# Kernel tuning notes

Hardware: AMD Instinct MI355X
Metric: run time of the kernel (lower is better)

The kernel has to match this reference:

```python
import jax, jax.numpy as jnp
import numpy as np
from jax import lax

EPS = 1e-5

def ste_sign(x):
    # forward-only module: plain sign is fine
    return jnp.sign(x)

def conv2d(x, w, pad):
    # x: NCHW, w: OIHW, stride 1
    return lax.conv_general_dilated(x, w, window_strides=(1, 1),
                                    padding=[(pad, pad), (pad, pad)],
                                    dimension_numbers=('NCHW', 'OIHW', 'NCHW'))

def maxpool2(x):
    # 2x2 max pool, stride 2, VALID (floor) -- matches nn.MaxPool2d(2,2)
    return lax.reduce_window(x, -jnp.inf, lax.max, (1, 1, 2, 2), (1, 1, 2, 2), 'VALID')

def batchnorm(x, gamma, beta):
    # training-mode BN: batch statistics over (N,H,W), biased variance
    mean = jnp.mean(x, axis=(0, 2, 3), keepdims=True)
    var = jnp.var(x, axis=(0, 2, 3), keepdims=True)
    xn = (x - mean) * lax.rsqrt(var + EPS)
    return xn * gamma[None, :, None, None] + beta[None, :, None, None]

def setup_inputs() -> dict:
    key = jax.random.key(0)
    ks = jax.random.split(key, 8)
    def he(k, shape):
        n = shape[2] * shape[3] * shape[0]
        return jax.random.normal(k, shape, jnp.float32) * np.sqrt(2.0 / n)
    x = jax.random.normal(ks[0], (4096, 1, 28, 28), jnp.float32)
    w0 = he(ks[1], (32, 1, 3, 3))
    w1 = he(ks[2], (32, 32, 3, 3))
    w2 = he(ks[3], (32, 32, 3, 3))
    g0 = jnp.ones((32,), jnp.float32); b0 = jnp.zeros((32,), jnp.float32)
    g1 = jnp.ones((32,), jnp.float32); b1 = jnp.zeros((32,), jnp.float32)
    g2 = jnp.ones((32,), jnp.float32); b2 = jnp.zeros((32,), jnp.float32)
    fw = jax.random.normal(ks[4], (10, 288), jnp.float32) * 0.01
    fb = jnp.zeros((10,), jnp.float32)
    return {"x": x, "w0": w0, "g0": g0, "b0": b0, "w1": w1, "g1": g1, "b1": b1,
            "w2": w2, "g2": g2, "b2": b2, "fw": fw, "fb": fb}

def reference(x, w0, g0, b0, w1, g1, b1, w2, g2, b2, fw, fb):
    # block0: fp conv -> pool -> bn (no act)
    h = batchnorm(maxpool2(conv2d(x, w0, 1)), g0, b0)          # [B,32,14,14]
    # block1: binary(1w1a) conv -> pool -> bn + maxpool(shortcut)
    o = batchnorm(maxpool2(conv2d(ste_sign(h), ste_sign(w1), 1)), g1, b1)
    h = o + maxpool2(h)                                         # [B,32,7,7]
    # block2
    o = batchnorm(maxpool2(conv2d(ste_sign(h), ste_sign(w2), 1)), g2, b2)
    h = o + maxpool2(h)                                         # [B,32,3,3]
    h = h.reshape(h.shape[0], -1)                                # [B,288]
    return h @ fw.T + fb                                         # [B,10]
```

## Files before the change

### kernel.cpp

```cpp
#include <hip/hip_runtime.h>
#include <stdint.h>

#define BATCH 4096

typedef float v16f __attribute__((ext_vector_type(16)));
typedef short v8s  __attribute__((ext_vector_type(8)));

__device__ __forceinline__ int sgn8(float v) {
    return (v > 0.f) ? 1 : ((v < 0.f) ? -1 : 0);
}

__global__ void k_signw1(const float* __restrict__ w, uint16_t* __restrict__ o) {
    int i = blockIdx.x * 256 + threadIdx.x;
    if (i >= 9216) return;
    int j = i & 7, n = (i >> 3) & 31, q = (i >> 8) & 1, kh = (i >> 9) & 1, tp = i >> 10;
    int cin = kh * 16 + q * 8 + j;
    float v = w[(n * 32 + cin) * 9 + tp];
    o[i] = (v > 0.f) ? 0x3F80 : ((v < 0.f) ? 0xBF80 : 0);
}

__global__ __launch_bounds__(448) void k_conv0s(const float* __restrict__ x,
                                                const float* __restrict__ w0,
                                                double* __restrict__ part0) {
    __shared__ float xs[960];
    __shared__ float wl[288];
    __shared__ double rs[32][14], rq[32][14];
    int n = blockIdx.x, t = threadIdx.x;
    for (int i = t; i < 960; i += 448) xs[i] = 0.f;
    for (int i = t; i < 288; i += 448) wl[i] = w0[i];
    __syncthreads();
    for (int i = t; i < 784; i += 448) {
        int y = i / 28, xx = i - y * 28;
        xs[(y + 1) * 32 + xx + 1] = x[n * 784 + i];
    }
    __syncthreads();
    int c = t & 31, py = t >> 5;
    float wreg[9];
    #pragma unroll
    for (int i = 0; i < 9; ++i) wreg[i] = wl[c * 9 + i];
    const float4* X4 = (const float4*)xs;
    float4 cur0 = X4[(2 * py + 0) * 8];
    float4 cur1 = X4[(2 * py + 1) * 8];
    float4 cur2 = X4[(2 * py + 2) * 8];
    float4 cur3 = X4[(2 * py + 3) * 8];
    double s = 0.0, q = 0.0;
    #pragma unroll
    for (int k = 0; k < 7; ++k) {
        float4 n0 = X4[(2 * py + 0) * 8 + k + 1];
        float4 n1 = X4[(2 * py + 1) * 8 + k + 1];
        float4 n2 = X4[(2 * py + 2) * 8 + k + 1];
        float4 n3 = X4[(2 * py + 3) * 8 + k + 1];
        float a[4][6];
        a[0][0] = cur0.x; a[0][1] = cur0.y; a[0][2] = cur0.z; a[0][3] = cur0.w; a[0][4] = n0.x; a[0][5] = n0.y;
        a[1][0] = cur1.x; a[1][1] = cur1.y; a[1][2] = cur1.z; a[1][3] = cur1.w; a[1][4] = n1.x; a[1][5] = n1.y;
        a[2][0] = cur2.x; a[2][1] = cur2.y; a[2][2] = cur2.z; a[2][3] = cur2.w; a[2][4] = n2.x; a[2][5] = n2.y;
        a[3][0] = cur3.x; a[3][1] = cur3.y; a[3][2] = cur3.z; a[3][3] = cur3.w; a[3][4] = n3.x; a[3][5] = n3.y;
        #pragma unroll
        for (int e = 0; e < 2; ++e) {
            int base = 2 * e;
            float s00 = 0.f, s01 = 0.f, s10 = 0.f, s11 = 0.f;
            #pragma unroll
            for (int ky = 0; ky < 3; ++ky)
            #pragma unroll
            for (int kx = 0; kx < 3; ++kx) {
                float w = wreg[ky * 3 + kx];
                s00 = fmaf(a[ky][base + kx], w, s00);
                s01 = fmaf(a[ky][base + kx + 1], w, s01);
                s10 = fmaf(a[ky + 1][base + kx], w, s10);
                s11 = fmaf(a[ky + 1][base + kx + 1], w, s11);
            }
            float m = fmaxf(fmaxf(s00, s01), fmaxf(s10, s11));
            double v = (double)m;
            s += v; q += v * v;
        }
        cur0 = n0; cur1 = n1; cur2 = n2; cur3 = n3;
    }
    rs[c][py] = s; rq[c][py] = q;
    __syncthreads();
    if (t < 32) {
        double S = 0.0, Q = 0.0;
        #pragma unroll
        for (int i = 0; i < 14; ++i) { S += rs[t][i]; Q += rq[t][i]; }
        part0[(size_t)t * 4096 + n] = S;
        part0[(size_t)32 * 4096 + (size_t)t * 4096 + n] = Q;
    }
}

__global__ __launch_bounds__(256) void k_finalize(const double* __restrict__ part, int G,
                                                  const float* __restrict__ g,
                                                  const float* __restrict__ b,
                                                  double inv_count, float* __restrict__ ss) {
    int c = blockIdx.x, t = threadIdx.x;
    double s = 0.0, q = 0.0;
    for (int i = t; i < G; i += 256) {
        s += part[(size_t)c * G + i];
        q += part[(size_t)32 * G + (size_t)c * G + i];
    }
    #pragma unroll
    for (int o = 32; o > 0; o >>= 1) { s += __shfl_down(s, o); q += __shfl_down(q, o); }
    __shared__ double rs[4], rq[4];
    int w = t >> 6, l = t & 63;
    if (l == 0) { rs[w] = s; rq[w] = q; }
    __syncthreads();
    if (t == 0) {
        s = rs[0] + rs[1] + rs[2] + rs[3];
        q = rq[0] + rq[1] + rq[2] + rq[3];
        double mean = s * inv_count;
        double var = q * inv_count - mean * mean;
        double sc = (double)g[c] / sqrt(var + 1e-5);
        ss[c] = (float)sc;
        ss[32 + c] = (float)((double)b[c] - mean * sc);
    }
}

__global__ __launch_bounds__(448) void k_bn0r(const float* __restrict__ x,
                                              const float* __restrict__ w0,
                                              const float* __restrict__ ss,
                                              uint32_t* __restrict__ s0b,
                                              float* __restrict__ hp0) {
    __shared__ float xs[960];
    __shared__ float wl[288];
    __shared__ float P[6468];
    int n = blockIdx.x, t = threadIdx.x;
    for (int i = t; i < 960; i += 448) xs[i] = 0.f;
    for (int i = t; i < 288; i += 448) wl[i] = w0[i];
    __syncthreads();
    for (int i = t; i < 784; i += 448) {
        int y = i / 28, xx = i - y * 28;
        xs[(y + 1) * 32 + xx + 1] = x[n * 784 + i];
    }
    __syncthreads();
    int c = t & 31, py = t >> 5;
    float wreg[9];
    #pragma unroll
    for (int i = 0; i < 9; ++i) wreg[i] = wl[c * 9 + i];
    float sc = ss[c], sh = ss[32 + c];
    const float4* X4 = (const float4*)xs;
    float4 cur0 = X4[(2 * py + 0) * 8];
    float4 cur1 = X4[(2 * py + 1) * 8];
    float4 cur2 = X4[(2 * py + 2) * 8];
    float4 cur3 = X4[(2 * py + 3) * 8];
    #pragma unroll
    for (int k = 0; k < 7; ++k) {
        float4 n0 = X4[(2 * py + 0) * 8 + k + 1];
        float4 n1 = X4[(2 * py + 1) * 8 + k + 1];
        float4 n2 = X4[(2 * py + 2) * 8 + k + 1];
        float4 n3 = X4[(2 * py + 3) * 8 + k + 1];
        float a[4][6];
        a[0][0] = cur0.x; a[0][1] = cur0.y; a[0][2] = cur0.z; a[0][3] = cur0.w; a[0][4] = n0.x; a[0][5] = n0.y;
        a[1][0] = cur1.x; a[1][1] = cur1.y; a[1][2] = cur1.z; a[1][3] = cur1.w; a[1][4] = n1.x; a[1][5] = n1.y;
        a[2][0] = cur2.x; a[2][1] = cur2.y; a[2][2] = cur2.z; a[2][3] = cur2.w; a[2][4] = n2.x; a[2][5] = n2.y;
        a[3][0] = cur3.x; a[3][1] = cur3.y; a[3][2] = cur3.z; a[3][3] = cur3.w; a[3][4] = n3.x; a[3][5] = n3.y;
        #pragma unroll
        for (int e = 0; e < 2; ++e) {
            int base = 2 * e;
            float s00 = 0.f, s01 = 0.f, s10 = 0.f, s11 = 0.f;
            #pragma unroll
            for (int ky = 0; ky < 3; ++ky)
            #pragma unroll
            for (int kx = 0; kx < 3; ++kx) {
                float w = wreg[ky * 3 + kx];
                s00 = fmaf(a[ky][base + kx], w, s00);
                s01 = fmaf(a[ky][base + kx + 1], w, s01);
                s10 = fmaf(a[ky + 1][base + kx], w, s10);
                s11 = fmaf(a[ky + 1][base + kx + 1], w, s11);
            }
            float m = fmaxf(fmaxf(s00, s01), fmaxf(s10, s11));
            P[(py * 14 + 2 * k + e) * 33 + c] = fmaf(sc, m, sh);
        }
        cur0 = n0; cur1 = n1; cur2 = n2; cur3 = n3;
    }
    __syncthreads();
    uint32_t* simg = s0b + (size_t)n * 4096;
    for (int i = t; i < 784; i += 448) {
        int pl = i >> 2, qd = i & 3;
        int iy = pl / 14, ix = pl - iy * 14;
        int yy = iy + 1, xx2 = ix + 1;
        int p = yy * 16 + xx2;
        int psw = (xx2 & 3) ^ (yy & 3);
        int g = qd ^ psw;
        const float* Pp = &P[pl * 33 + g * 8];
        uint32_t d[4];
        #pragma unroll
        for (int j = 0; j < 4; ++j) {
            float h0 = Pp[2 * j], h1 = Pp[2 * j + 1];
            uint32_t b0 = (h0 > 0.f) ? 0x3F80u : ((h0 < 0.f) ? 0xBF80u : 0u);
            uint32_t b1 = (h1 > 0.f) ? 0x3F80u : ((h1 < 0.f) ? 0xBF80u : 0u);
            d[j] = b0 | (b1 << 16);
        }
        uint4 v; v.x = d[0]; v.y = d[1]; v.z = d[2]; v.w = d[3];
        *(uint4*)(simg + p * 16 + qd * 4) = v;
    }
    if (t < 240) {
        int e = t >> 2, qd = t & 3;
        int yh, xh;
        if (e < 16)      { yh = 0;      xh = e; }
        else if (e < 32) { yh = 15;     xh = e - 16; }
        else if (e < 46) { yh = e - 31; xh = 0; }
        else             { yh = e - 45; xh = 15; }
        uint4 z; z.x = z.y = z.z = z.w = 0u;
        *(uint4*)(simg + (yh * 16 + xh) * 16 + qd * 4) = z;
    }
    if (t < 196) {
        int pw = t >> 2, oct = t & 3;
        int pyy = pw / 7, pxx = pw - pyy * 7;
        int b00 = ((2 * pyy) * 14 + 2 * pxx) * 33;
        int b01 = b00 + 33;
        int b10 = b00 + 14 * 33;
        int b11 = b10 + 33;
        float out[8];
        #pragma unroll
        for (int k = 0; k < 8; ++k) {
            int cc = oct * 8 + k;
            out[k] = fmaxf(fmaxf(P[b00 + cc], P[b01 + cc]),
                           fmaxf(P[b10 + cc], P[b11 + cc]));
        }
        float4* hd = (float4*)(hp0 + ((size_t)n * 49 + pw) * 32 + oct * 8);
        float4 h0; h0.x = out[0]; h0.y = out[1]; h0.z = out[2]; h0.w = out[3];
        float4 h1; h1.x = out[4]; h1.y = out[5]; h1.z = out[6]; h1.w = out[7];
        hd[0] = h0; hd[1] = h1;
    }
}

__global__ __launch_bounds__(256) void k_conv1m(const uint32_t* __restrict__ s0b,
                                                const uint16_t* __restrict__ w1f,
                                                float* __restrict__ p1,
                                                double* __restrict__ part1) {
    __shared__ uint32_t lds[8192];
    int t = threadIdx.x;
    int n0 = blockIdx.x * 2;
    const uint4* gp = (const uint4*)(s0b + (size_t)n0 * 4096);
    uint4* lp = (uint4*)lds;
    #pragma unroll
    for (int i = 0; i < 8; ++i) lp[t + i * 256] = gp[t + i * 256];
    int lane = t & 63, wv = t >> 6;
    int q = lane >> 5, ncol = lane & 31;
    v8s wfr[18];
    #pragma unroll
    for (int f = 0; f < 18; ++f)
        wfr[f] = *(const v8s*)(w1f + (f * 2 + q) * 256 + ncol * 8);
    __syncthreads();
    int img = wv >> 1, wh = wv & 1;
    int n = n0 + img;
    int ibase = img * 4096;
    int m = lane & 31;
    int quad = m & 3, pwl = m >> 2;
    int dy = quad >> 1, dx = quad & 1;
    double sAcc = 0.0, qAcc = 0.0;
    for (int tile = wh; tile < 7; tile += 2) {
        int pw = tile * 8 + pwl;
        int pwc = min(pw, 48);
        int py = pwc / 7, px = pwc - py * 7;
        int pbase = (2 * py + dy) * 16 + 2 * px + dx;
        v16f acc;
        #pragma unroll
        for (int i = 0; i < 16; ++i) acc[i] = 0.f;
        #pragma unroll
        for (int tp = 0; tp < 9; ++tp) {
            int p = pbase + (tp / 3) * 16 + (tp % 3);
            int psw = (p ^ (p >> 4)) & 3;
            #pragma unroll
            for (int kh = 0; kh < 2; ++kh) {
                int g = kh * 2 + q;
                int idx = ibase + p * 16 + ((g ^ psw) << 2);
                v8s a = *(const v8s*)&lds[idx];
                acc = __builtin_amdgcn_mfma_f32_32x32x16_bf16(a, wfr[tp * 2 + kh], acc, 0, 0, 0);
            }
        }
        #pragma unroll
        for (int g4 = 0; g4 < 4; ++g4) {
            float mx = fmaxf(fmaxf(acc[4 * g4], acc[4 * g4 + 1]),
                             fmaxf(acc[4 * g4 + 2], acc[4 * g4 + 3]));
            int pwo = tile * 8 + 2 * g4 + q;
            if (pwo < 49) {
                p1[((size_t)n * 49 + pwo) * 32 + ncol] = mx;
                double v = (double)mx;
                sAcc += v; qAcc += v * v;
            }
        }
    }
    __syncthreads();
    double* red = (double*)lds;
    red[(wv * 2 + q) * 32 + ncol] = sAcc;
    red[256 + (wv * 2 + q) * 32 + ncol] = qAcc;
    __syncthreads();
    if (t < 32) {
        double S = 0.0, Q = 0.0;
        #pragma unroll
        for (int i = 0; i < 8; ++i) { S += red[i * 32 + t]; Q += red[256 + i * 32 + t]; }
        part1[(size_t)t * 2048 + blockIdx.x] = S;
        part1[(size_t)32 * 2048 + (size_t)t * 2048 + blockIdx.x] = Q;
    }
}

__global__ __launch_bounds__(256) void k_bn1(const float* __restrict__ p1,
                                             const float* __restrict__ hp0,
                                             const float* __restrict__ ss,
                                             uint32_t* __restrict__ s1,
                                             float* __restrict__ hp1) {
    __shared__ float H[1568];
    int n = blockIdx.x, t = threadIdx.x;
    const float* P = p1 + (size_t)n * 1568;
    const float* Hp = hp0 + (size_t)n * 1568;
    for (int i = t; i < 1568; i += 256) {
        int c = i & 31;
        H[i] = fmaf(ss[64 + c], P[i], ss[96 + c]) + Hp[i];
    }
    __syncthreads();
    if (t < 32) {
        int c = t;
        uint32_t* sp = s1 + (size_t)n * 416 + c * 13;
        for (int j = 0; j < 13; ++j) {
            uint32_t u = 0;
            #pragma unroll
            for (int k = 0; k < 4; ++k) {
                int f = 4 * j + k;
                int sv = (f < 49) ? sgn8(H[f * 32 + c]) : 0;
                u |= ((uint32_t)(uint8_t)(int8_t)sv) << (8 * k);
            }
            sp[j] = u;
        }
    }
    for (int jj = t; jj < 288; jj += 256) {
        int c = jj / 9, pix = jj - c * 9;
        int r = pix / 3, qq = pix - r * 3;
        float a0 = H[((2 * r) * 7 + 2 * qq) * 32 + c];
        float a1 = H[((2 * r) * 7 + 2 * qq + 1) * 32 + c];
        float a2 = H[((2 * r + 1) * 7 + 2 * qq) * 32 + c];
        float a3 = H[((2 * r + 1) * 7 + 2 * qq + 1) * 32 + c];
        hp1[n * 288 + c * 9 + pix] = fmaxf(fmaxf(a0, a1), fmaxf(a2, a3));
    }
}

__global__ __launch_bounds__(256) void k_conv2m(const uint32_t* __restrict__ s1,
                                                const uint16_t* __restrict__ w2f,
                                                float* __restrict__ p2,
                                                double* __restrict__ part2) {
    __shared__ uint32_t lds[8192];
    int t = threadIdx.x;
    int n0 = blockIdx.x * 8;
    for (int i = t; i < 120; i += 256) {
        int img = i / 15, e = i - img * 15;
        int p = (e < 8) ? e : (e - 7) * 8;
        uint32_t* d = &lds[img * 1024 + p * 16];
        uint4 z; z.x = z.y = z.z = z.w = 0u;
        ((uint4*)d)[0] = z; ((uint4*)d)[1] = z; ((uint4*)d)[2] = z; ((uint4*)d)[3] = z;
    }
    int lane = t & 63, wv = t >> 6;
    int q = lane >> 5, ncol = lane & 31;
    v8s wfr[18];
    #pragma unroll
    for (int f = 0; f < 18; ++f)
        wfr[f] = *(const v8s*)(w2f + (f * 2 + q) * 256 + ncol * 8);
    for (int i = t; i < 1664; i += 256) {
        int img = i / 208, r = i - img * 208;
        int c2 = r / 13, j = r - c2 * 13;
        const uint32_t* sb = s1 + (size_t)(n0 + img) * 416;
        uint32_t wa = sb[(2 * c2) * 13 + j];
        uint32_t wb = sb[(2 * c2 + 1) * 13 + j];
        int g = c2 >> 2, sub = c2 & 3;
        #pragma unroll
        for (int k = 0; k < 4; ++k) {
            int f = 4 * j + k;
            if (f < 49) {
                int y = f / 7, x = f - y * 7;
                int p = (y + 1) * 8 + (x + 1);
                uint32_t ba = (wa >> (8 * k)) & 0xFF;
                uint32_t bb = (wb >> (8 * k)) & 0xFF;
                uint32_t ha = ba ? (0x3F80u | ((ba & 0x80u) << 8)) : 0u;
                uint32_t hb = bb ? (0x3F80u | ((bb & 0x80u) << 8)) : 0u;
                lds[img * 1024 + p * 16 + ((g ^ (p & 3)) << 2) + sub] = ha | (hb << 16);
            }
        }
    }
    __syncthreads();
    int m = lane & 31;
    int quad = m & 3, pwl = m >> 2;
    int dy = quad >> 1, dx = quad & 1;
    double sAcc = 0.0, qAcc = 0.0;
    for (int tile = wv; tile < 9; tile += 4) {
        int pwg = tile * 8 + pwl;
        int img = pwg / 9, pwi = pwg - img * 9;
        int py = pwi / 3, px = pwi - py * 3;
        int pbase = (2 * py + dy) * 8 + 2 * px + dx;
        v16f acc;
        #pragma unroll
        for (int i = 0; i < 16; ++i) acc[i] = 0.f;
        #pragma unroll
        for (int tp = 0; tp < 9; ++tp) {
            int p = pbase + (tp / 3) * 8 + (tp % 3);
            int psw = p & 3;
            #pragma unroll
            for (int kh = 0; kh < 2; ++kh) {
                int g = kh * 2 + q;
                int idx = img * 1024 + p * 16 + ((g ^ psw) << 2);
                v8s a = *(const v8s*)&lds[idx];
                acc = __builtin_amdgcn_mfma_f32_32x32x16_bf16(a, wfr[tp * 2 + kh], acc, 0, 0, 0);
            }
        }
        #pragma unroll
        for (int g4 = 0; g4 < 4; ++g4) {
            float mx = fmaxf(fmaxf(acc[4 * g4], acc[4 * g4 + 1]),
                             fmaxf(acc[4 * g4 + 2], acc[4 * g4 + 3]));
            int pwo = tile * 8 + 2 * g4 + q;
            int oimg = pwo / 9, opwi = pwo - oimg * 9;
            p2[(size_t)(n0 + oimg) * 288 + ncol * 9 + opwi] = mx;
            double v = (double)mx;
            sAcc += v; qAcc += v * v;
        }
    }
    __syncthreads();
    double* red = (double*)lds;
    red[(wv * 2 + q) * 32 + ncol] = sAcc;
    red[256 + (wv * 2 + q) * 32 + ncol] = qAcc;
    __syncthreads();
    if (t < 32) {
        double S = 0.0, Q = 0.0;
        #pragma unroll
        for (int i = 0; i < 8; ++i) { S += red[i * 32 + t]; Q += red[256 + i * 32 + t]; }
        part2[(size_t)t * 512 + blockIdx.x] = S;
        part2[(size_t)32 * 512 + (size_t)t * 512 + blockIdx.x] = Q;
    }
}

__global__ __launch_bounds__(256) void k_fc(const float* __restrict__ p2,
                                            const float* __restrict__ hp1,
                                            const float* __restrict__ ss,
                                            const float* __restrict__ fw,
                                            const float* __restrict__ fb,
                                            float* __restrict__ outv) {
    int wv = threadIdx.x >> 6, l = threadIdx.x & 63;
    int n = blockIdx.x * 4 + wv;
    float acc[10];
    #pragma unroll
    for (int k = 0; k < 10; ++k) acc[k] = 0.f;
    #pragma unroll
    for (int i = 0; i < 5; ++i) {
        int j = l + 64 * i;
        if (j < 288) {
            int c = j / 9;
            float h = fmaf(ss[128 + c], p2[n * 288 + j], ss[160 + c]) + hp1[n * 288 + j];
            #pragma unroll
            for (int k = 0; k < 10; ++k)
                acc[k] = fmaf(h, fw[k * 288 + j], acc[k]);
        }
    }
    #pragma unroll
    for (int k = 0; k < 10; ++k) {
        float s = acc[k];
        #pragma unroll
        for (int o = 32; o > 0; o >>= 1) s += __shfl_down(s, o);
        if (l == 0) outv[n * 10 + k] = s + fb[k];
    }
}

extern "C" void kernel_launch(void* const* d_in, const int* in_sizes, int n_in,
                              void* d_out, int out_size, void* d_ws, size_t ws_size,
                              hipStream_t stream) {
    (void)in_sizes; (void)n_in; (void)out_size; (void)ws_size;
    const float* x  = (const float*)d_in[0];
    const float* w0 = (const float*)d_in[1];
    const float* g0 = (const float*)d_in[2];
    const float* b0 = (const float*)d_in[3];
    const float* w1 = (const float*)d_in[4];
    const float* g1 = (const float*)d_in[5];
    const float* b1 = (const float*)d_in[6];
    const float* w2 = (const float*)d_in[7];
    const float* g2 = (const float*)d_in[8];
    const float* b2 = (const float*)d_in[9];
    const float* fw = (const float*)d_in[10];
    const float* fb = (const float*)d_in[11];
    float* outv = (float*)d_out;
    char* ws = (char*)d_ws;

    float*     ss    = (float*)(ws + 1024);
    uint16_t*  w1f   = (uint16_t*)(ws + 2048);
    uint16_t*  w2f   = (uint16_t*)(ws + 38912);
    float*     p1    = (float*)(ws + 76800);
    uint32_t*  s1    = (uint32_t*)(ws + 25766912);
    float*     hp1   = (float*)(ws + 32582656);
    float*     p2    = (float*)(ws + 37301248);
    uint32_t*  s0b   = (uint32_t*)(ws + 42019840);
    double*    part0 = (double*)(ws + 109128704);
    double*    part1 = (double*)(ws + 111225856);
    double*    part2 = (double*)(ws + 112274432);
    float*     hp0   = (float*)(ws + 128527360);

    k_signw1<<<36, 256, 0, stream>>>(w1, w1f);
    k_signw1<<<36, 256, 0, stream>>>(w2, w2f);

    k_conv0s<<<BATCH, 448, 0, stream>>>(x, w0, part0);
    k_finalize<<<32, 256, 0, stream>>>(part0, 4096, g0, b0, 1.0 / (BATCH * 196.0), ss);
    k_bn0r<<<BATCH, 448, 0, stream>>>(x, w0, ss, s0b, hp0);

    k_conv1m<<<BATCH / 2, 256, 0, stream>>>(s0b, w1f, p1, part1);
    k_finalize<<<32, 256, 0, stream>>>(part1, 2048, g1, b1, 1.0 / (BATCH * 49.0), ss + 64);
    k_bn1<<<BATCH, 256, 0, stream>>>(p1, hp0, ss, s1, hp1);

    k_conv2m<<<BATCH / 8, 256, 0, stream>>>(s1, w2f, p2, part2);
    k_finalize<<<32, 256, 0, stream>>>(part2, 512, g2, b2, 1.0 / (BATCH * 9.0), ss + 128);

    k_fc<<<BATCH / 4, 256, 0, stream>>>(p2, hp1, ss, fw, fb, outv);
}
```

Measured before the change: 217.9 us.

## Fold BN finalize into conv kernels via last-block atomic ticket

Drops the three separate finalize launches and the two weight-sign launches. The weight-sign work moves into the first conv kernel, and each conv kernel's last block, found with an atomic counter, computes the BN scale and shift. This cuts launch and serialization overhead, but the final statistics reduction now runs on a single block, looping over 32 channels serially with syncs. It also adds a memset to clear the counters.

After: 667.1 us. 3.06x slower.

```diff
diff --git a/kernel.cpp b/kernel.cpp
--- a/kernel.cpp
+++ b/kernel.cpp
@@ -10,22 +10,65 @@
     return (v > 0.f) ? 1 : ((v < 0.f) ? -1 : 0);
 }
 
-__global__ void k_signw1(const float* __restrict__ w, uint16_t* __restrict__ o) {
-    int i = blockIdx.x * 256 + threadIdx.x;
-    if (i >= 9216) return;
-    int j = i & 7, n = (i >> 3) & 31, q = (i >> 8) & 1, kh = (i >> 9) & 1, tp = i >> 10;
-    int cin = kh * 16 + q * 8 + j;
-    float v = w[(n * 32 + cin) * 9 + tp];
-    o[i] = (v > 0.f) ? 0x3F80 : ((v < 0.f) ? 0xBF80 : 0);
+__device__ void finalize_all(const double* __restrict__ part, int G,
+                             const float* __restrict__ g, const float* __restrict__ b,
+                             double inv_count, float* __restrict__ ssout,
+                             int t, double* red) {
+    for (int c = 0; c < 32; ++c) {
+        double s = 0.0, q = 0.0;
+        if (t < 256) {
+            for (int i = t; i < G; i += 256) {
+                s += part[(size_t)c * G + i];
+                q += part[(size_t)32 * G + (size_t)c * G + i];
+            }
+        }
+        #pragma unroll
+        for (int o = 32; o > 0; o >>= 1) { s += __shfl_down(s, o); q += __shfl_down(q, o); }
+        int w = t >> 6, l = t & 63;
+        if (l == 0 && w < 4) { red[w] = s; red[8 + w] = q; }
+        __syncthreads();
+        if (t == 0) {
+            s = red[0] + red[1] + red[2] + red[3];
+            q = red[8] + red[9] + red[10] + red[11];
+            double mean = s * inv_count;
+            double var = q * inv_count - mean * mean;
+            double sc = (double)g[c] / sqrt(var + 1e-5);
+            ssout[c] = (float)sc;
+            ssout[32 + c] = (float)((double)b[c] - mean * sc);
+        }
+        __syncthreads();
+    }
 }
 
 __global__ __launch_bounds__(448) void k_conv0s(const float* __restrict__ x,
                                                 const float* __restrict__ w0,
-                                                double* __restrict__ part0) {
+                                                const float* __restrict__ w1,
+                                                const float* __restrict__ w2,
+                                                const float* __restrict__ g0,
+                                                const float* __restrict__ b0,
+                                                uint16_t* __restrict__ w1f,
+                                                uint16_t* __restrict__ w2f,
+                                                double* __restrict__ part0,
+                                                float* __restrict__ ss,
+                                                uint32_t* __restrict__ counter) {
     __shared__ float xs[960];
     __shared__ float wl[288];
-    __shared__ double rs[32][14], rq[32][14];
+    __shared__ double rs[448], rq[448];
+    __shared__ double red[16];
+    __shared__ int isLast;
     int n = blockIdx.x, t = threadIdx.x;
+
+    if (n < 72 && t < 256) {
+        int i = n * 256 + t;
+        int ii = (i < 9216) ? i : i - 9216;
+        const float* w = (i < 9216) ? w1 : w2;
+        uint16_t* o = (i < 9216) ? w1f : w2f;
+        int j = ii & 7, nn = (ii >> 3) & 31, q2 = (ii >> 8) & 1, kh = (ii >> 9) & 1, tp = ii >> 10;
+        int cin = kh * 16 + q2 * 8 + j;
+        float v = w[(nn * 32 + cin) * 9 + tp];
+        o[ii] = (v > 0.f) ? 0x3F80 : ((v < 0.f) ? 0xBF80 : 0);
+    }
+
     for (int i = t; i < 960; i += 448) xs[i] = 0.f;
     for (int i = t; i < 288; i += 448) wl[i] = w0[i];
     __syncthreads();
@@ -75,41 +118,25 @@
         }
         cur0 = n0; cur1 = n1; cur2 = n2; cur3 = n3;
     }
-    rs[c][py] = s; rq[c][py] = q;
+    rs[c * 14 + py] = s; rq[c * 14 + py] = q;
     __syncthreads();
     if (t < 32) {
         double S = 0.0, Q = 0.0;
         #pragma unroll
-        for (int i = 0; i < 14; ++i) { S += rs[t][i]; Q += rq[t][i]; }
+        for (int i = 0; i < 14; ++i) { S += rs[t * 14 + i]; Q += rq[t * 14 + i]; }
         part0[(size_t)t * 4096 + n] = S;
         part0[(size_t)32 * 4096 + (size_t)t * 4096 + n] = Q;
-    }
-}
-
-__global__ __launch_bounds__(256) void k_finalize(const double* __restrict__ part, int G,
-                                                  const float* __restrict__ g,
-                                                  const float* __restrict__ b,
-                                                  double inv_count, float* __restrict__ ss) {
-    int c = blockIdx.x, t = threadIdx.x;
-    double s = 0.0, q = 0.0;
-    for (int i = t; i < G; i += 256) {
-        s += part[(size_t)c * G + i];
-        q += part[(size_t)32 * G + (size_t)c * G + i];
-    }
-    #pragma unroll
-    for (int o = 32; o > 0; o >>= 1) { s += __shfl_down(s, o); q += __shfl_down(q, o); }
-    __shared__ double rs[4], rq[4];
-    int w = t >> 6, l = t & 63;
-    if (l == 0) { rs[w] = s; rq[w] = q; }
+        __threadfence();
+    }
     __syncthreads();
     if (t == 0) {
-        s = rs[0] + rs[1] + rs[2] + rs[3];
-        q = rq[0] + rq[1] + rq[2] + rq[3];
-        double mean = s * inv_count;
-        double var = q * inv_count - mean * mean;
-        double sc = (double)g[c] / sqrt(var + 1e-5);
-        ss[c] = (float)sc;
-        ss[32 + c] = (float)((double)b[c] - mean * sc);
+        uint32_t ticket = atomicAdd(counter, 1u);
+        isLast = (ticket == (uint32_t)(gridDim.x - 1));
+    }
+    __syncthreads();
+    if (isLast) {
+        __threadfence();
+        finalize_all(part0, 4096, g0, b0, 1.0 / (4096.0 * 196.0), ss, t, red);
     }
 }
 
@@ -224,9 +251,14 @@
 
 __global__ __launch_bounds__(256) void k_conv1m(const uint32_t* __restrict__ s0b,
                                                 const uint16_t* __restrict__ w1f,
+                                                const float* __restrict__ g1,
+                                                const float* __restrict__ b1,
                                                 float* __restrict__ p1,
-                                                double* __restrict__ part1) {
+                                                double* __restrict__ part1,
+                                                float* __restrict__ ss,
+                                                uint32_t* __restrict__ counter) {
     __shared__ uint32_t lds[8192];
+    __shared__ int isLast;
     int t = threadIdx.x;
     int n0 = blockIdx.x * 2;
     const uint4* gp = (const uint4*)(s0b + (size_t)n0 * 4096);
@@ -290,6 +322,17 @@
         for (int i = 0; i < 8; ++i) { S += red[i * 32 + t]; Q += red[256 + i * 32 + t]; }
         part1[(size_t)t * 2048 + blockIdx.x] = S;
         part1[(size_t)32 * 2048 + (size_t)t * 2048 + blockIdx.x] = Q;
+        __threadfence();
+    }
+    __syncthreads();
+    if (t == 0) {
+        uint32_t ticket = atomicAdd(counter, 1u);
+        isLast = (ticket == (uint32_t)(gridDim.x - 1));
+    }
+    __syncthreads();
+    if (isLast) {
+        __threadfence();
+        finalize_all(part1, 2048, g1, b1, 1.0 / (4096.0 * 49.0), ss + 64, t, red + 512);
     }
 }
 
@@ -334,9 +377,14 @@
 
 __global__ __launch_bounds__(256) void k_conv2m(const uint32_t* __restrict__ s1,
                                                 const uint16_t* __restrict__ w2f,
+                                                const float* __restrict__ g2,
+                                                const float* __restrict__ b2,
                                                 float* __restrict__ p2,
-                                                double* __restrict__ part2) {
+                                                double* __restrict__ part2,
+                                                float* __restrict__ ss,
+                                                uint32_t* __restrict__ counter) {
     __shared__ uint32_t lds[8192];
+    __shared__ int isLast;
     int t = threadIdx.x;
     int n0 = blockIdx.x * 8;
     for (int i = t; i < 120; i += 256) {
@@ -363,8 +411,8 @@
         for (int k = 0; k < 4; ++k) {
             int f = 4 * j + k;
             if (f < 49) {
-                int y = f / 7, x = f - y * 7;
-                int p = (y + 1) * 8 + (x + 1);
+                int y = f / 7, xq = f - y * 7;
+                int p = (y + 1) * 8 + (xq + 1);
                 uint32_t ba = (wa >> (8 * k)) & 0xFF;
                 uint32_t bb = (wb >> (8 * k)) & 0xFF;
                 uint32_t ha = ba ? (0x3F80u | ((ba & 0x80u) << 8)) : 0u;
@@ -420,6 +468,17 @@
         for (int i = 0; i < 8; ++i) { S += red[i * 32 + t]; Q += red[256 + i * 32 + t]; }
         part2[(size_t)t * 512 + blockIdx.x] = S;
         part2[(size_t)32 * 512 + (size_t)t * 512 + blockIdx.x] = Q;
+        __threadfence();
+    }
+    __syncthreads();
+    if (t == 0) {
+        uint32_t ticket = atomicAdd(counter, 1u);
+        isLast = (ticket == (uint32_t)(gridDim.x - 1));
+    }
+    __syncthreads();
+    if (isLast) {
+        __threadfence();
+        finalize_all(part2, 512, g2, b2, 1.0 / (4096.0 * 9.0), ss + 128, t, red + 512);
     }
 }
 
@@ -473,6 +532,7 @@
     float* outv = (float*)d_out;
     char* ws = (char*)d_ws;
 
+    uint32_t*  ctr   = (uint32_t*)(ws + 0);
     float*     ss    = (float*)(ws + 1024);
     uint16_t*  w1f   = (uint16_t*)(ws + 2048);
     uint16_t*  w2f   = (uint16_t*)(ws + 38912);
@@ -486,19 +546,16 @@
     double*    part2 = (double*)(ws + 112274432);
     float*     hp0   = (float*)(ws + 128527360);
 
-    k_signw1<<<36, 256, 0, stream>>>(w1, w1f);
-    k_signw1<<<36, 256, 0, stream>>>(w2, w2f);
-
-    k_conv0s<<<BATCH, 448, 0, stream>>>(x, w0, part0);
-    k_finalize<<<32, 256, 0, stream>>>(part0, 4096, g0, b0, 1.0 / (BATCH * 196.0), ss);
+    hipMemsetAsync(ctr, 0, 64, stream);
+
+    k_conv0s<<<BATCH, 448, 0, stream>>>(x, w0, w1, w2, g0, b0, w1f, w2f,
+                                        part0, ss, ctr + 0);
     k_bn0r<<<BATCH, 448, 0, stream>>>(x, w0, ss, s0b, hp0);
 
-    k_conv1m<<<BATCH / 2, 256, 0, stream>>>(s0b, w1f, p1, part1);
-    k_finalize<<<32, 256, 0, stream>>>(part1, 2048, g1, b1, 1.0 / (BATCH * 49.0), ss + 64);
+    k_conv1m<<<BATCH / 2, 256, 0, stream>>>(s0b, w1f, g1, b1, p1, part1, ss, ctr + 1);
     k_bn1<<<BATCH, 256, 0, stream>>>(p1, hp0, ss, s1, hp1);
 
-    k_conv2m<<<BATCH / 8, 256, 0, stream>>>(s1, w2f, p2, part2);
-    k_finalize<<<32, 256, 0, stream>>>(part2, 512, g2, b2, 1.0 / (BATCH * 9.0), ss + 128);
+    k_conv2m<<<BATCH / 8, 256, 0, stream>>>(s1, w2f, g2, b2, p2, part2, ss, ctr + 2);
 
     k_fc<<<BATCH / 4, 256, 0, stream>>>(p2, hp1, ss, fw, fb, outv);
 }
```
